# Performance work log

Hardware: AMD Instinct MI355X
Metric: run time of the kernel (lower is better)

Reference implementation:

```python
import jax, jax.numpy as jnp
import numpy as np

B, N, T, IN_DIM, OUT_DIM = 16, 500, 12, 2, 2
H, D, K, NH, NBLOCKS, T_OUT, GDEP = 64, 64, 10, 24, 2, 12, 2
H2 = 2 * H


def setup_inputs():
    key = jax.random.key(0)
    ks = iter(jax.random.split(key, 64))

    def rn(shape, s=1.0):
        return jax.random.normal(next(ks), shape, dtype=jnp.float32) * s

    def z(*shape):
        return jnp.zeros(shape, jnp.float32)

    sI = 1.0 / np.sqrt(IN_DIM)
    sH = 1.0 / np.sqrt(H)
    sH2 = 1.0 / np.sqrt(H2)
    sD = 1.0 / np.sqrt(D)
    adj = jax.random.uniform(next(ks), (N, N), dtype=jnp.float32)
    inp = {
        'x': rn((B, N, T, IN_DIM)),
        'weather': rn((B, T, 4)),
        'geo_adj': adj / adj.sum(1, keepdims=True),
        'fcx_W': rn((IN_DIM, H), sI), 'fcx_b': z(H),
        'env_cb': rn((K, D)), 'nodes_cb': rn((N, D)),
        'w_v': rn((D, K), sD), 'w_k': rn((D, D), sD), 'w_q': rn((D, D), sD),
        'core_W': rn((H, H * H), sH), 'core_b': z(H * H),
        'tcnN_Win': rn((K, H2, H2), sH2), 'tcnN_bin': z(K, H2),
        'tcnN_Wf': rn((K, NBLOCKS, 2, H2, H2), sH2), 'tcnN_bf': z(K, NBLOCKS, H2),
        'tcnN_Wg': rn((K, NBLOCKS, 2, H2, H2), sH2), 'tcnN_bg': z(K, NBLOCKS, H2),
        'tcnN_Wout': rn((K, H2, H), sH2), 'tcnN_bout': z(K, H),
        'tcnP_Win': rn((K, H2, H2), sH2), 'tcnP_bin': z(K, H2),
        'tcnP_Wf': rn((K, NBLOCKS, 2, H2, H2), sH2), 'tcnP_bf': z(K, NBLOCKS, H2),
        'tcnP_Wg': rn((K, NBLOCKS, 2, H2, H2), sH2), 'tcnP_bg': z(K, NBLOCKS, H2),
        'tcnP_Wout': rn((K, H2, H), sH2), 'tcnP_bout': z(K, H),
        'bn1_g': jnp.ones((H,), jnp.float32), 'bn1_b': z(H),
        'bnP_g': jnp.ones((H,), jnp.float32), 'bnP_b': z(H),
        'gcn1_W': rn((H, H), sH), 'gcn1_b': z(H),
        'gcn2_W': rn((H, H), sH), 'gcn2_b': z(H),
        'gcnp_W': rn((H, H), sH), 'gcnp_b': z(H),
        'nv_p1': rn((2 * NH, H)), 'nv_p2': rn((N, H)), 'nv_p3': rn((N, H)),
        'nv_pk': rn((H, H, H), sH),
        'out_W1': rn((T_OUT, H, 100), sH), 'out_b1': z(T_OUT, 100),
        'out_W2': rn((T_OUT, 100, OUT_DIM), 0.1), 'out_b2': z(T_OUT, OUT_DIM),
        't_pos': jax.random.randint(next(ks), (B, T, 2), 0, 7),
        'ind': jax.random.randint(next(ks), (B, T, 2), 0, 7),
    }
    return inp


def _tstep_emb(t, dim):
    half = dim // 2
    freqs = jnp.exp(-jnp.log(10000.0) * jnp.arange(half, dtype=jnp.float32) / half)
    a = t.astype(jnp.float32)[:, None] * freqs[None]
    return jnp.concatenate([jnp.cos(a), jnp.sin(a)], -1)


def _conv2(h, W, b, d):
    # causal kernel-2 dilated conv over time: h [B,N,T,C], W [2,C,Co] -> [B,N,T-d,Co]
    return (jnp.einsum('bntc,co->bnto', h[:, :, :-d], W[0])
            + jnp.einsum('bntc,co->bnto', h[:, :, d:], W[1]) + b)


def _tcn(xin, Win, bin_, Wf, bf, Wg, bg, Wout, bout):
    # gated dilated TCN (Graph-WaveNet style), per node over time
    h = jnp.einsum('bntc,co->bnto', xin, Win) + bin_
    for l in range(Wf.shape[0]):
        d = 2 ** l
        f = jnp.tanh(_conv2(h, Wf[l], bf[l], d))
        g = jax.nn.sigmoid(_conv2(h, Wg[l], bg[l], d))
        h = f * g + h[:, :, d:, :]
    return jnp.einsum('bntc,ch->bnth', h, Wout) + bout


def _bn(h, g, b):
    # BatchNorm1d over channels, stats over (batch, nodes); training mode
    mu = h.mean((0, 1))
    var = h.var((0, 1))
    return g * (h - mu) * jax.lax.rsqrt(var + 1e-5) + b


def _gcn(h, adj, W, b):
    # multi-hop diffusion: sum_{k=0..GDEP} A^k h, then linear
    eq = 'nm,bmh->bnh' if adj.ndim == 2 else 'bnm,bmh->bnh'
    acc, zt = h, h
    for _ in range(GDEP):
        zt = jnp.einsum(eq, adj, zt)
        acc = acc + zt
    return jnp.einsum('bnh,ho->bno', acc, W) + b


def _forward(x, weather, geo_adj, fcx_W, fcx_b, env_cb, nodes_cb, w_v, w_k, w_q,
             core_W, core_b,
             tcnN_Win, tcnN_bin, tcnN_Wf, tcnN_bf, tcnN_Wg, tcnN_bg, tcnN_Wout, tcnN_bout,
             tcnP_Win, tcnP_bin, tcnP_Wf, tcnP_bf, tcnP_Wg, tcnP_bg, tcnP_Wout, tcnP_bout,
             bn1_g, bn1_b, bnP_g, bnP_b, gcn1_W, gcn1_b, gcn2_W, gcn2_b, gcnp_W, gcnp_b,
             nv_p1, nv_p2, nv_p3, nv_pk, out_W1, out_b1, out_W2, out_b2, t_pos, ind):
    scale = 1.0 / jnp.sqrt(jnp.float32(D))
    ind_p = jnp.where(ind[:, :, 0] <= 4, ind[:, :, 1], NH - 1 + ind[:, :, 1])
    tp = jnp.where(t_pos[:, :, 0] <= 4, t_pos[:, :, 1], NH - 1 + t_pos[:, :, 1])
    t_emb = _tstep_emb(tp.reshape(-1), H).reshape(B, T, H)

    # codebook attention -> hard cluster assignment (gumbel softmax, straight-through)
    mat_v = env_cb @ w_v
    mat_k = env_cb @ w_k
    mat_q = nodes_cb @ w_q
    scores = jax.nn.softmax((mat_q @ mat_k.T) * scale, axis=1)
    logits = scores @ mat_v                                   # [N,K]
    gn = jax.random.gumbel(jax.random.key(42), logits.shape, dtype=logits.dtype)
    y_soft = jax.nn.softmax(logits + gn, axis=1)
    hard = jax.nn.one_hot(jnp.argmax(y_soft, axis=1), K, dtype=y_soft.dtype)
    mask = y_soft + jax.lax.stop_gradient(hard - y_soft)      # [N,K] one-hot fwd

    x_emb = jnp.einsum('bnti,ih->bnth', x, fcx_W) + fcx_b
    total_x = jnp.concatenate(
        [x_emb, jnp.broadcast_to(t_emb[:, None], (B, N, T, H))], -1)  # [B,N,T,2H]

    unbias = jnp.zeros((B, N, H), total_x.dtype)
    h_prev = jnp.zeros((B, N, H), total_x.dtype)
    for i in range(K):  # small fixed cluster count
        m = mask[:, i]
        xm = total_x * m[None, :, None, None]
        hn = _tcn(xm[:, :, 1:], tcnN_Win[i], tcnN_bin[i], tcnN_Wf[i], tcnN_bf[i],
                  tcnN_Wg[i], tcnN_bg[i], tcnN_Wout[i], tcnN_bout[i])[:, :, 0, :]
        hp = _tcn(xm[:, :, :-1], tcnP_Win[i], tcnP_bin[i], tcnP_Wf[i], tcnP_bf[i],
                  tcnP_Wg[i], tcnP_bg[i], tcnP_Wout[i], tcnP_bout[i])[:, :, 0, :]
        unbias = unbias + m[None, :, None] * hn
        h_prev = h_prev + m[None, :, None] * hp

    unbias = _bn(unbias, bn1_g, bn1_b)
    h_prev = _bn(h_prev, bnP_g, bnP_b)

    h1 = _gcn(h_prev, geo_adj, gcn1_W, gcn1_b)
    core = (t_emb[:, T - 1] @ core_W + core_b).reshape(B, H, H)
    causal = jax.nn.softmax(jnp.einsum('bnh,bhk,bmk->bnm', unbias, core, h_prev), axis=-1)
    h2 = _gcn(unbias, causal, gcn2_W, gcn2_b)

    te = nv_p1[ind_p[:, -(T - 1)]]                            # [B,H]
    adp = jnp.einsum('ai,ijk->ajk', te, nv_pk)
    adp = jnp.einsum('bj,ajk->abk', nv_p2, adp)
    adp = jnp.einsum('ck,abk->abc', nv_p3, adp)
    adp = jax.nn.softmax(jax.nn.relu(adp), axis=2)            # [B,N,N]
    h3 = _gcn(unbias, adp, gcnp_W, gcnp_b)

    cur_h = h1 + h2 + h3
    hmid = jax.nn.elu(jnp.einsum('bnh,thf->bntf', cur_h, out_W1) + out_b1)
    return jnp.einsum('bntf,tfo->bnto', hmid, out_W2) + out_b2  # [B,N,T_OUT,OUT_DIM]


def reference(x, weather, geo_adj, fcx_W, fcx_b, env_cb, nodes_cb, w_v, w_k, w_q,
              core_W, core_b,
              tcnN_Win, tcnN_bin, tcnN_Wf, tcnN_bf, tcnN_Wg, tcnN_bg, tcnN_Wout, tcnN_bout,
              tcnP_Win, tcnP_bin, tcnP_Wf, tcnP_bf, tcnP_Wg, tcnP_bg, tcnP_Wout, tcnP_bout,
              bn1_g, bn1_b, bnP_g, bnP_b, gcn1_W, gcn1_b, gcn2_W, gcn2_b, gcnp_W, gcnp_b,
              nv_p1, nv_p2, nv_p3, nv_pk, out_W1, out_b1, out_W2, out_b2, t_pos, ind):
    return _forward(x, weather, geo_adj, fcx_W, fcx_b, env_cb, nodes_cb, w_v, w_k, w_q,
                    core_W, core_b,
                    tcnN_Win, tcnN_bin, tcnN_Wf, tcnN_bf, tcnN_Wg, tcnN_bg, tcnN_Wout, tcnN_bout,
                    tcnP_Win, tcnP_bin, tcnP_Wf, tcnP_bf, tcnP_Wg, tcnP_bg, tcnP_Wout, tcnP_bout,
                    bn1_g, bn1_b, bnP_g, bnP_b, gcn1_W, gcn1_b, gcn2_W, gcn2_b, gcnp_W, gcnp_b,
                    nv_p1, nv_p2, nv_p3, nv_pk, out_W1, out_b1, out_W2, out_b2, t_pos, ind)
```

## Files before the change

kernel.cpp:

```cpp
#include <hip/hip_runtime.h>
#include <hip/hip_bf16.h>
#include <math.h>

#define B_ 16
#define N_ 500
#define T_ 12
#define K_ 10
#define NROWS (B_*N_)
#define TROWS 6

__device__ __forceinline__ unsigned rotl32(unsigned v, int r){ return (v<<r)|(v>>(32-r)); }

__device__ __forceinline__ void threefry2x32(unsigned k0, unsigned k1,
                                             unsigned c0, unsigned c1,
                                             unsigned &o0, unsigned &o1){
  unsigned ks2 = k0 ^ k1 ^ 0x1BD11BDAu;
  unsigned x0 = c0 + k0, x1 = c1 + k1;
#define TF_R(r) { x0 += x1; x1 = rotl32(x1,(r)); x1 ^= x0; }
  TF_R(13) TF_R(15) TF_R(26) TF_R(6)
  x0 += k1;  x1 += ks2 + 1u;
  TF_R(17) TF_R(29) TF_R(16) TF_R(24)
  x0 += ks2; x1 += k0 + 2u;
  TF_R(13) TF_R(15) TF_R(26) TF_R(6)
  x0 += k0;  x1 += k1 + 3u;
// ... 481 lines not shown
    #pragma unroll
    for (int ii=0;ii<3;++ii){
      int i = ig + ii;
      float f = tanhf(af[ii] + bfv);
      float g = 1.f/(1.f + expf(-(ag[ii] + bgv)));
      sH2[i*128 + o] = f*g + sH1[(i*2+1)*128 + o];
    }
  }
  __syncthreads();

  {
    int o6 = tid & 63, grp = tid >> 6;
    #pragma unroll
    for (int ii=0; ii<2; ++ii){
      int i = grp*2 + ii;
      if (i >= TROWS) continue;
      float acc = 0.f;
      for (int c = 0; c < 128; c += 4){
        float w0=Wout[(c+0)*64+o6], w1=Wout[(c+1)*64+o6],
              w2=Wout[(c+2)*64+o6], w3=Wout[(c+3)*64+o6];
        float4 xv = *(const float4*)&sH2[i*128 + c];
        acc += xv.x*w0 + xv.y*w1 + xv.z*w2 + xv.w*w3;
      }
      if (rowBN[i] >= 0) outb[rowBN[i]*64 + o6] = acc + bout[o6];
    }
  }
}

__global__ __launch_bounds__(256) void k_bnstats(const float* __restrict__ unb,
                                                 const float* __restrict__ hpr,
                                                 float* __restrict__ stats){
  int bid = blockIdx.x;
  int tensor = bid >> 6, c = bid & 63;
  const float* buf = tensor ? hpr : unb;
  float s1 = 0.f, s2 = 0.f;
  for (int r = threadIdx.x; r < NROWS; r += 256){
    float v = buf[r*64 + c];
    s1 += v; s2 += v*v;
  }
  __shared__ float r1[256], r2[256];
  r1[threadIdx.x]=s1; r2[threadIdx.x]=s2;
  __syncthreads();
  for (int s=128; s>0; s>>=1){
    if (threadIdx.x < s){ r1[threadIdx.x]+=r1[threadIdx.x+s]; r2[threadIdx.x]+=r2[threadIdx.x+s]; }
    __syncthreads();
  }
  if (threadIdx.x==0){
    float mean = r1[0]/(float)NROWS;
    float var  = r2[0]/(float)NROWS - mean*mean;
    stats[tensor*128 + c]      = mean;
    stats[tensor*128 + 64 + c] = rsqrtf(var + 1e-5f);
  }
}

__global__ __launch_bounds__(256) void k_bnapply(float* __restrict__ unb, float* __restrict__ hpr,
                                                 const float* __restrict__ stats,
                                                 const float* __restrict__ g1, const float* __restrict__ be1,
                                                 const float* __restrict__ gP, const float* __restrict__ beP){
  int idx = blockIdx.x*256 + threadIdx.x;
  if (idx >= 2*NROWS*64) return;
  int tensor = idx >= NROWS*64;
  int local = idx - tensor*NROWS*64;
  int c = local & 63;
  float* buf = tensor ? hpr : unb;
  float mean = stats[tensor*128+c], rstd = stats[tensor*128+64+c];
  float g = tensor ? gP[c] : g1[c];
  float bb = tensor ? beP[c] : be1[c];
  buf[local] = g * (buf[local]-mean) * rstd + bb;
}

template<int AMODE, int RELU, int FINAL, int ADD>
__global__ __launch_bounds__(256) void k_attn(
    const float* __restrict__ geo,
    const float* __restrict__ Qf, const float* __restrict__ Qb,
    const float* __restrict__ M,
    const float* __restrict__ Keysf, const float* __restrict__ Keysb,
    const float* __restrict__ X,
    const float* __restrict__ X0, const float* __restrict__ Z1,
    const float* __restrict__ Wg, const float* __restrict__ bg,
    float* __restrict__ cur, float* __restrict__ Y)
{
  __shared__ __align__(16) float kbuf[64][65];
  __shared__ __align__(16) float xbuf[64][64];
  __shared__ __align__(16) float vbuf[8][64];
  __shared__ __align__(16) float pbuf[8][64];

  int b = blockIdx.y, n0 = blockIdx.x*8;
  int tid = threadIdx.x;
  int nl = tid >> 5, ml = tid & 31;
  int n = n0 + nl;
  float rrK[16], rrX[16], rrA[2];

  if (AMODE != 0){
    for (int idx = tid; idx < 512; idx += 256){
      int r = idx >> 6, kk = idx & 63;
      int nn = n0 + r;
      float q = 0.f;
      if (nn < N_) q = (AMODE == 1) ? Qf[(b*N_+nn)*64+kk] : Qb[nn*64+kk];
      pbuf[r][kk] = q;
    }
    for (int idx = tid; idx < 4096; idx += 256)
      kbuf[idx>>6][idx&63] = M[b*4096 + idx];
    __syncthreads();
    float vx = 0.f, vy = 0.f;
    for (int kk = 0; kk < 64; ++kk){
      float q = pbuf[nl][kk];
      float2 m2 = *(const float2*)&kbuf[kk][ml*2];
      vx += q*m2.x; vy += q*m2.y;
    }
    __syncthreads();
    vbuf[nl][ml*2]   = vx;
    vbuf[nl][ml*2+1] = vy;
  }
  {
    if (AMODE != 0) __syncthreads();
    #pragma unroll
    for (int ii = 0; ii < 16; ++ii){
      int idx = tid + ii*256;
      int mm = idx >> 6, kk = idx & 63;
      if (AMODE != 0)
        kbuf[mm][kk] = (AMODE == 1) ? Keysf[(b*N_+mm)*64+kk] : Keysb[mm*64+kk];
      xbuf[mm][kk] = X[(b*N_+mm)*64+kk];
    }
    if (AMODE == 0){
      #pragma unroll
      for (int ii = 0; ii < 2; ++ii){
        int idx = tid + ii*256;
        int r = idx >> 6, mm = idx & 63;
        int nn = n0 + r;
        pbuf[r][mm] = (nn < N_) ? geo[nn*N_ + mm] : 0.f;
      }
    }
    __syncthreads();
  }

  float m_run = -1e30f, l_run = 0.f;
  float accx = 0.f, accy = 0.f;

  for (int ci = 0; ci < 8; ++ci){
    int m0 = ci*64;
    if (ci < 7){
      #pragma unroll
      for (int ii=0; ii<16; ++ii){
        int idx = tid + ii*256;
        int mm = idx >> 6, kk = idx & 63;
        int m = m0 + 64 + mm;
        if (AMODE != 0)
          rrK[ii] = (m < N_) ? ((AMODE == 1) ? Keysf[(b*N_+m)*64+kk] : Keysb[m*64+kk]) : 0.f;
        rrX[ii] = (m < N_) ? X[(b*N_+m)*64+kk] : 0.f;
      }
      if (AMODE == 0){
        #pragma unroll
        for (int ii=0; ii<2; ++ii){
          int idx = tid + ii*256;
          int r = idx >> 6, mm = idx & 63;
          int nn = n0 + r, m = m0 + 64 + mm;
          rrA[ii] = (nn < N_ && m < N_) ? geo[nn*N_ + m] : 0.f;
        }
      }
    }
    if (AMODE != 0){
      float s0 = 0.f, s1 = 0.f;
      for (int kk = 0; kk < 64; kk += 4){
        float4 qv = *(const float4*)&vbuf[nl][kk];
        float4 k0 = *(const float4*)&kbuf[ml   ][kk];
        float4 k1 = *(const float4*)&kbuf[ml+32][kk];
        s0 += qv.x*k0.x + qv.y*k0.y + qv.z*k0.z + qv.w*k0.w;
        s1 += qv.x*k1.x + qv.y*k1.y + qv.z*k1.z + qv.w*k1.w;
      }
      float v0 = (m0 + ml      < N_) ? (RELU ? fmaxf(s0, 0.f) : s0) : -1e30f;
      float v1 = (m0 + ml + 32 < N_) ? (RELU ? fmaxf(s1, 0.f) : s1) : -1e30f;
      float cmax = fmaxf(v0, v1);
      #pragma unroll
      for (int msk = 1; msk < 32; msk <<= 1) cmax = fmaxf(cmax, __shfl_xor(cmax, msk, 32));
      float mnew = fmaxf(m_run, cmax);
      float scale = expf(m_run - mnew);
      float p0 = expf(v0 - mnew);
      float p1 = expf(v1 - mnew);
      float lc = p0 + p1;
      #pragma unroll
      for (int msk = 1; msk < 32; msk <<= 1) lc += __shfl_xor(lc, msk, 32);
      l_run = l_run*scale + lc;
      m_run = mnew;
      accx *= scale; accy *= scale;
      pbuf[nl][ml]    = p0;
      pbuf[nl][ml+32] = p1;
    }
    __syncthreads();
    for (int mm = 0; mm < 64; mm += 4){
      float4 pv = *(const float4*)&pbuf[nl][mm];
      float2 x0 = *(const float2*)&xbuf[mm+0][ml*2];
      float2 x1 = *(const float2*)&xbuf[mm+1][ml*2];
      float2 x2 = *(const float2*)&xbuf[mm+2][ml*2];
      float2 x3 = *(const float2*)&xbuf[mm+3][ml*2];
      accx += pv.x*x0.x + pv.y*x1.x + pv.z*x2.x + pv.w*x3.x;
      accy += pv.x*x0.y + pv.y*x1.y + pv.z*x2.y + pv.w*x3.y;
    }
    __syncthreads();
    if (ci < 7){
      #pragma unroll
      for (int ii=0; ii<16; ++ii){
        int idx = tid + ii*256;
        int mm = idx >> 6, kk = idx & 63;
        if (AMODE != 0) kbuf[mm][kk] = rrK[ii];
        xbuf[mm][kk] = rrX[ii];
      }
      if (AMODE == 0){
        #pragma unroll
        for (int ii=0; ii<2; ++ii){
          int idx = tid + ii*256;
          pbuf[idx>>6][idx&63] = rrA[ii];
        }
      }
      __syncthreads();
    }
  }
  if (AMODE != 0){
    float inv = 1.f / l_run;
    accx *= inv; accy *= inv;
  }

  if (!FINAL){
    if (n < N_){
      float2 o2; o2.x = accx; o2.y = accy;
      *(float2*)&Y[(b*N_+n)*64 + ml*2] = o2;
    }
    return;
  }

  {
    int row = b*N_ + n;
    float svx = 0.f, svy = 0.f;
    if (n < N_){
      float2 x0v = *(const float2*)&X0[row*64 + ml*2];
      float2 z1v = *(const float2*)&Z1[row*64 + ml*2];
      svx = accx + x0v.x + z1v.x;
      svy = accy + x0v.y + z1v.y;
    }
    vbuf[nl][ml*2]   = svx;
    vbuf[nl][ml*2+1] = svy;
    for (int idx = tid; idx < 4096; idx += 256)
      kbuf[idx>>6][idx&63] = Wg[idx];
    __syncthreads();
    float ox = 0.f, oy = 0.f;
    for (int kk = 0; kk < 64; ++kk){
      float s = vbuf[nl][kk];
      float2 w2 = *(const float2*)&kbuf[kk][ml*2];
      ox += s*w2.x; oy += s*w2.y;
    }
    if (n < N_){
      float2 bv = *(const float2*)&bg[ml*2];
      float vx = ox + bv.x, vy = oy + bv.y;
      if (ADD){
        float2 old = *(const float2*)&cur[row*64 + ml*2];
        vx += old.x; vy += old.y;
      }
      float2 o2; o2.x = vx; o2.y = vy;
      *(float2*)&cur[row*64 + ml*2] = o2;
    }
  }
}

template<int AMODE, int RELU>
__global__ __launch_bounds__(256) void k_attn_p1(
    const float* __restrict__ Qf, const float* __restrict__ Qb,
    const float* __restrict__ M,
    const float* __restrict__ Keysf, const float* __restrict__ Keysb,
    const float* __restrict__ X,
    float* __restrict__ Pb, float* __restrict__ Y)
{
  __shared__ __align__(16) float kbuf[64][65];
  __shared__ __align__(16) float xbuf[64][64];
  __shared__ __align__(16) float vbuf[8][64];
  __shared__ __align__(16) float pbuf[8][64];

  int b = blockIdx.y, n0 = blockIdx.x*8;
  int tid = threadIdx.x;
  int nl = tid >> 5, ml = tid & 31;
  int n = n0 + nl;
  float rrK[16], rrX[16];

  for (int idx = tid; idx < 512; idx += 256){
    int r = idx >> 6, kk = idx & 63;
    int nn = n0 + r;
    float q = 0.f;
    if (nn < N_) q = (AMODE == 1) ? Qf[(b*N_+nn)*64+kk] : Qb[nn*64+kk];
    pbuf[r][kk] = q;
  }
  for (int idx = tid; idx < 4096; idx += 256)
    kbuf[idx>>6][idx&63] = M[b*4096 + idx];
  __syncthreads();
  float vx = 0.f, vy = 0.f;
  for (int kk = 0; kk < 64; ++kk){
    float q = pbuf[nl][kk];
    float2 m2 = *(const float2*)&kbuf[kk][ml*2];
    vx += q*m2.x; vy += q*m2.y;
  }
  __syncthreads();
  vbuf[nl][ml*2]   = vx;
  vbuf[nl][ml*2+1] = vy;
  __syncthreads();
  #pragma unroll
  for (int ii = 0; ii < 16; ++ii){
    int idx = tid + ii*256;
    int mm = idx >> 6, kk = idx & 63;
    kbuf[mm][kk] = (AMODE == 1) ? Keysf[(b*N_+mm)*64+kk] : Keysb[mm*64+kk];
    xbuf[mm][kk] = X[(b*N_+mm)*64+kk];
  }
  __syncthreads();

  float m_run = -1e30f, l_run = 0.f;
  float accx = 0.f, accy = 0.f;

  for (int ci = 0; ci < 8; ++ci){
    int m0 = ci*64;
    if (ci < 7){
      #pragma unroll
      for (int ii=0; ii<16; ++ii){
        int idx = tid + ii*256;
        int mm = idx >> 6, kk = idx & 63;
        int m = m0 + 64 + mm;
        rrK[ii] = (m < N_) ? ((AMODE == 1) ? Keysf[(b*N_+m)*64+kk] : Keysb[m*64+kk]) : 0.f;
        rrX[ii] = (m < N_) ? X[(b*N_+m)*64+kk] : 0.f;
      }
    }
    {
      float s0 = 0.f, s1 = 0.f;
      for (int kk = 0; kk < 64; kk += 4){
        float4 qv = *(const float4*)&vbuf[nl][kk];
        float4 k0 = *(const float4*)&kbuf[ml   ][kk];
        float4 k1 = *(const float4*)&kbuf[ml+32][kk];
        s0 += qv.x*k0.x + qv.y*k0.y + qv.z*k0.z + qv.w*k0.w;
        s1 += qv.x*k1.x + qv.y*k1.y + qv.z*k1.z + qv.w*k1.w;
      }
      float v0 = (m0 + ml      < N_) ? (RELU ? fmaxf(s0, 0.f) : s0) : -1e30f;
      float v1 = (m0 + ml + 32 < N_) ? (RELU ? fmaxf(s1, 0.f) : s1) : -1e30f;
      if (n < N_){
        Pb[((long)(b*N_+n))*512 + m0 + ml]      = v0;
        Pb[((long)(b*N_+n))*512 + m0 + ml + 32] = v1;
      }
      float cmax = fmaxf(v0, v1);
      #pragma unroll
      for (int msk = 1; msk < 32; msk <<= 1) cmax = fmaxf(cmax, __shfl_xor(cmax, msk, 32));
      float mnew = fmaxf(m_run, cmax);
      float scale = expf(m_run - mnew);
      float p0 = expf(v0 - mnew);
      float p1 = expf(v1 - mnew);
      float lc = p0 + p1;
      #pragma unroll
      for (int msk = 1; msk < 32; msk <<= 1) lc += __shfl_xor(lc, msk, 32);
      l_run = l_run*scale + lc;
      m_run = mnew;
      accx *= scale; accy *= scale;
      pbuf[nl][ml]    = p0;
      pbuf[nl][ml+32] = p1;
    }
    __syncthreads();
    for (int mm = 0; mm < 64; mm += 4){
      float4 pv = *(const float4*)&pbuf[nl][mm];
      float2 x0 = *(const float2*)&xbuf[mm+0][ml*2];
      float2 x1 = *(const float2*)&xbuf[mm+1][ml*2];
      float2 x2 = *(const float2*)&xbuf[mm+2][ml*2];
      float2 x3 = *(const float2*)&xbuf[mm+3][ml*2];
      accx += pv.x*x0.x + pv.y*x1.x + pv.z*x2.x + pv.w*x3.x;
      accy += pv.x*x0.y + pv.y*x1.y + pv.z*x2.y + pv.w*x3.y;
    }
    __syncthreads();
    if (ci < 7){
      #pragma unroll
      for (int ii=0; ii<16; ++ii){
        int idx = tid + ii*256;
        kbuf[idx>>6][idx&63] = rrK[ii];
        xbuf[idx>>6][idx&63] = rrX[ii];
      }
      __syncthreads();
    }
  }
  float inv = 1.f / l_run;
  accx *= inv; accy *= inv;
  if (n < N_){
    float2 o2; o2.x = accx; o2.y = accy;
    *(float2*)&Y[(b*N_+n)*64 + ml*2] = o2;
  }
}

template<int ADD>
__global__ __launch_bounds__(256) void k_attn_p2(
    const float* __restrict__ Pb,
    const float* __restrict__ X,
    const float* __restrict__ X0,
    const float* __restrict__ Wg, const float* __restrict__ bg,
    float* __restrict__ cur)
{
  __shared__ __align__(16) float pbuf[8][516];
  __shared__ __align__(16) float xbuf[64][64];
  __shared__ __align__(16) float vbuf[8][64];

  int b = blockIdx.y, n0 = blockIdx.x*8;
  int tid = threadIdx.x;
  int nl = tid >> 5, ml = tid & 31;
  int n = n0 + nl;
  float rrX[16];

  for (int idx = tid; idx < 8*512; idx += 256){
    int r = idx >> 9, m = idx & 511;
    int nn = n0 + r;
    pbuf[r][m] = (nn < N_) ? Pb[((long)(b*N_+nn))*512 + m] : -1e30f;
  }
  __syncthreads();
  float lmax = -1e30f;
  for (int m = ml; m < 512; m += 32) lmax = fmaxf(lmax, pbuf[nl][m]);
  #pragma unroll
  for (int msk=1; msk<32; msk<<=1) lmax = fmaxf(lmax, __shfl_xor(lmax, msk, 32));
  float lsum = 0.f;
  for (int m = ml; m < 512; m += 32){
    float p = expf(pbuf[nl][m] - lmax);
    pbuf[nl][m] = p;
    lsum += p;
  }
  #pragma unroll
  for (int msk=1; msk<32; msk<<=1) lsum += __shfl_xor(lsum, msk, 32);
  float inv = 1.f/lsum;
  for (int m = ml; m < 512; m += 32) pbuf[nl][m] *= inv;

  #pragma unroll
  for (int ii=0; ii<16; ++ii){
    int idx = tid + ii*256;
    int mm = idx>>6, kk = idx&63;
    xbuf[mm][kk] = X[(b*N_+mm)*64+kk];
  }
  __syncthreads();

  float accx = 0.f, accy = 0.f;
  for (int ci = 0; ci < 8; ++ci){
    int m0 = ci*64;
    if (ci < 7){
      #pragma unroll
      for (int ii=0; ii<16; ++ii){
        int idx = tid + ii*256;
        int mm = idx>>6, kk = idx&63;
        int m = m0+64+mm;
        rrX[ii] = (m < N_) ? X[(b*N_+m)*64+kk] : 0.f;
      }
    }
    for (int mm = 0; mm < 64; mm += 4){
      float4 pv = *(const float4*)&pbuf[nl][m0+mm];
      float2 x0 = *(const float2*)&xbuf[mm+0][ml*2];
      float2 x1 = *(const float2*)&xbuf[mm+1][ml*2];
      float2 x2 = *(const float2*)&xbuf[mm+2][ml*2];
      float2 x3 = *(const float2*)&xbuf[mm+3][ml*2];
      accx += pv.x*x0.x + pv.y*x1.x + pv.z*x2.x + pv.w*x3.x;
      accy += pv.x*x0.y + pv.y*x1.y + pv.z*x2.y + pv.w*x3.y;
    }
    __syncthreads();
    if (ci < 7){
      #pragma unroll
      for (int ii=0; ii<16; ++ii){
        int idx = tid + ii*256;
        xbuf[idx>>6][idx&63] = rrX[ii];
      }
      __syncthreads();
    }
  }

  {
    int row = b*N_ + n;
    float svx = 0.f, svy = 0.f;
    if (n < N_){
      float2 x0v = *(const float2*)&X0[row*64 + ml*2];
      float2 z1v = *(const float2*)&X[row*64 + ml*2];
      svx = accx + x0v.x + z1v.x;
      svy = accy + x0v.y + z1v.y;
    }
    vbuf[nl][ml*2]   = svx;
    vbuf[nl][ml*2+1] = svy;
    for (int idx = tid; idx < 4096; idx += 256)
      xbuf[idx>>6][idx&63] = Wg[idx];
    __syncthreads();
    float ox = 0.f, oy = 0.f;
    for (int kk = 0; kk < 64; ++kk){
      float s = vbuf[nl][kk];
      float2 w2 = *(const float2*)&xbuf[kk][ml*2];
      ox += s*w2.x; oy += s*w2.y;
    }
    if (n < N_){
      float2 bv = *(const float2*)&bg[ml*2];
      float vx = ox + bv.x, vy = oy + bv.y;
      if (ADD){
        float2 old = *(const float2*)&cur[row*64 + ml*2];
        vx += old.x; vy += old.y;
      }
      float2 o2; o2.x = vx; o2.y = vy;
      *(float2*)&cur[row*64 + ml*2] = o2;
    }
  }
}

__global__ __launch_bounds__(128) void k_out(const float* __restrict__ cur,
                                             const float* __restrict__ W1, const float* __restrict__ bb1,
                                             const float* __restrict__ W2, const float* __restrict__ bb2,
                                             float* __restrict__ out){
  __shared__ float ch[4][64];
  __shared__ float hid[4*1200];
  int tid = threadIdx.x;
  int rbase = blockIdx.x*4;
  for (int idx = tid; idx < 256; idx += 128){
    int r = idx >> 6, h = idx & 63;
    ch[r][h] = cur[(rbase+r)*64 + h];
  }
  __syncthreads();
  for (int job = tid; job < 1200; job += 128){
    int t = job / 100, f = job - t*100;
    float a0 = bb1[t*100+f], a1 = a0, a2 = a0, a3 = a0;
    for (int h = 0; h < 64; ++h){
      float w = W1[(t*64+h)*100 + f];
      a0 += ch[0][h]*w; a1 += ch[1][h]*w; a2 += ch[2][h]*w; a3 += ch[3][h]*w;
    }
    hid[0*1200+job] = (a0 > 0.f) ? a0 : expm1f(a0);
    hid[1*1200+job] = (a1 > 0.f) ? a1 : expm1f(a1);
    hid[2*1200+job] = (a2 > 0.f) ? a2 : expm1f(a2);
    hid[3*1200+job] = (a3 > 0.f) ? a3 : expm1f(a3);
  }
  __syncthreads();
  if (tid < 96){
    int r = tid / 24, rem = tid % 24;
    int t = rem >> 1, o = rem & 1;
    float a = bb2[t*2+o];
    const float* hp = hid + r*1200 + t*100;
    for (int f = 0; f < 100; ++f) a += hp[f] * W2[(t*100+f)*2+o];
    out[(rbase+r)*24 + t*2+o] = a;
  }
}

extern "C" void kernel_launch(void* const* d_in, const int* in_sizes, int n_in,
                              void* d_out, int out_size, void* d_ws, size_t ws_size,
                              hipStream_t stream)
{
  const float* x        = (const float*)d_in[0];
  const float* geo      = (const float*)d_in[2];
  const float* fcx_W    = (const float*)d_in[3];
  const float* fcx_b    = (const float*)d_in[4];
  const float* env_cb   = (const float*)d_in[5];
  const float* nodes_cb = (const float*)d_in[6];
  const float* w_v      = (const float*)d_in[7];
  const float* w_k      = (const float*)d_in[8];
  const float* w_q      = (const float*)d_in[9];
  const float* core_W   = (const float*)d_in[10];
  const float* core_b   = (const float*)d_in[11];
  const float* tN_Win   = (const float*)d_in[12];
  const float* tN_bin   = (const float*)d_in[13];
  const float* tN_Wf    = (const float*)d_in[14];
  const float* tN_bf    = (const float*)d_in[15];
  const float* tN_Wg    = (const float*)d_in[16];
  const float* tN_bg    = (const float*)d_in[17];
  const float* tN_Wout  = (const float*)d_in[18];
  const float* tN_bout  = (const float*)d_in[19];
  const float* tP_Win   = (const float*)d_in[20];
  const float* tP_bin   = (const float*)d_in[21];
  const float* tP_Wf    = (const float*)d_in[22];
  const float* tP_bf    = (const float*)d_in[23];
  const float* tP_Wg    = (const float*)d_in[24];
  const float* tP_bg    = (const float*)d_in[25];
  const float* tP_Wout  = (const float*)d_in[26];
  const float* tP_bout  = (const float*)d_in[27];
  const float* bn1_g    = (const float*)d_in[28];
  const float* bn1_b    = (const float*)d_in[29];
  const float* bnP_g    = (const float*)d_in[30];
  const float* bnP_b    = (const float*)d_in[31];
  const float* gcn1_W   = (const float*)d_in[32];
  const float* gcn1_b   = (const float*)d_in[33];
  const float* gcn2_W   = (const float*)d_in[34];
  const float* gcn2_b   = (const float*)d_in[35];
  const float* gcnp_W   = (const float*)d_in[36];
  const float* gcnp_b   = (const float*)d_in[37];
  const float* nv_p1    = (const float*)d_in[38];
  const float* nv_p2    = (const float*)d_in[39];
  const float* nv_p3    = (const float*)d_in[40];
  const float* nv_pk    = (const float*)d_in[41];
  const float* out_W1   = (const float*)d_in[42];
  const float* out_b1   = (const float*)d_in[43];
  const float* out_W2   = (const float*)d_in[44];
  const float* out_b2   = (const float*)d_in[45];
  const int*   t_pos    = (const int*)d_in[46];
  const int*   ind      = (const int*)d_in[47];

  int* node_list = (int*)d_ws;
  int* off       = node_list + 512;
  float* F = (float*)((char*)d_ws + 4096);
  float* temb   = F + 0;
  float* core_f = F + 12288;
  float* tmp1   = F + 77824;
  float* stats  = F + 143360;
  float* matq   = F + 143616;
  float* unb    = F + 175616;
  float* hpr    = F + 687616;
  float* cur    = F + 1199616;
  float* zt1    = F + 1711616;
  float* Pb     = F + 2223616;
  float* TE     = Pb;
  bool useP = ws_size >= (size_t)(4096 + (size_t)(2223616 + 4096000)*4);

  k_matq <<<dim3(125), dim3(256), 0, stream>>>(nodes_cb, w_q, matq);
  k_route<<<dim3(1),   dim3(256), 0, stream>>>(env_cb, w_v, w_k, matq, node_list, off);
  k_temb <<<dim3(1),   dim3(192), 0, stream>>>(t_pos, temb);
  k_core <<<dim3(256), dim3(256), 0, stream>>>(temb, core_W, core_b, core_f);
  if (useP){
    k_tprep<<<dim3(20, 81), dim3(128), 0, stream>>>(temb, fcx_W, fcx_b, tN_Win, tP_Win, TE);
    k_tcn2 <<<dim3(20, 334), dim3(256), 0, stream>>>(x, TE, node_list, off,
        tN_bin, tN_Wf, tN_bf, tN_Wg, tN_bg, tN_Wout, tN_bout,
        tP_bin, tP_Wf, tP_bf, tP_Wg, tP_bg, tP_Wout, tP_bout,
        unb, hpr);
  } else {
    k_tcn  <<<dim3(20, 334), dim3(256), 0, stream>>>(x, fcx_W, fcx_b, temb, node_list, off,
        tN_Win, tN_bin, tN_Wf, tN_bf, tN_Wg, tN_bg, tN_Wout, tN_bout,
        tP_Win, tP_bin, tP_Wf, tP_bf, tP_Wg, tP_bg, tP_Wout, tP_bout,
        unb, hpr);
  }
  k_bnstats<<<dim3(128), dim3(256), 0, stream>>>(unb, hpr, stats);
  k_bnapply<<<dim3(4000),dim3(256), 0, stream>>>(unb, hpr, stats, bn1_g, bn1_b, bnP_g, bnP_b);
  k_tmp1<<<dim3(256), dim3(256), 0, stream>>>(ind, nv_p1, nv_pk, tmp1);

  dim3 ag(64, 16);
  const float* nil = nullptr;
  k_attn<0,0,0,0><<<ag, 256, 0, stream>>>(geo, nil,nil,nil, nil,nil,
                                 hpr, nil,nil, nil,nil, nullptr, zt1);
  k_attn<0,0,1,0><<<ag, 256, 0, stream>>>(geo, nil,nil,nil, nil,nil,
                                 zt1, hpr, zt1, gcn1_W, gcn1_b, cur, nullptr);
  if (useP){
    k_attn_p1<1,0><<<ag, 256, 0, stream>>>(unb, nil, core_f, hpr, nil, unb, Pb, zt1);
    k_attn_p2<1>  <<<ag, 256, 0, stream>>>(Pb, zt1, unb, gcn2_W, gcn2_b, cur);
  } else {
    k_attn<1,0,0,0><<<ag, 256, 0, stream>>>(nil, unb,nil, core_f, hpr,nil,
                                   unb, nil,nil, nil,nil, nullptr, zt1);
    k_attn<1,0,1,1><<<ag, 256, 0, stream>>>(nil, unb,nil, core_f, hpr,nil,
                                   zt1, unb, zt1, gcn2_W, gcn2_b, cur, nullptr);
  }
  if (useP){
    k_attn_p1<2,1><<<ag, 256, 0, stream>>>(nil, nv_p2, tmp1, nil, nv_p3, unb, Pb, zt1);
    k_attn_p2<1>  <<<ag, 256, 0, stream>>>(Pb, zt1, unb, gcnp_W, gcnp_b, cur);
  } else {
    k_attn<2,1,0,0><<<ag, 256, 0, stream>>>(nil, nil,nv_p2, tmp1, nil,nv_p3,
                                   unb, nil,nil, nil,nil, nullptr, zt1);
    k_attn<2,1,1,1><<<ag, 256, 0, stream>>>(nil, nil,nv_p2, tmp1, nil,nv_p3,
                                   zt1, unb, zt1, gcnp_W, gcnp_b, cur, nullptr);
  }
  k_out<<<dim3(2000), dim3(128), 0, stream>>>(cur, out_W1, out_b1, out_W2, out_b2, (float*)d_out);
}
```

Baseline: 950.8 us.

## Process two query rows per warp in attention kernels to reuse key/value tiles

Each block of the attention kernels (k_attn, k_attn_p1, k_attn_p2) now covers 16 query nodes instead of 8, with every warp handling two rows (A and B). This halves the grid and reuses each staged key/X chunk from shared memory for twice as many queries, which cuts global loads of keys and values per output. In exchange it raises register pressure and shared memory per block and launches fewer blocks (32x16), which may lower occupancy.

```diff
diff --git a/kernel.cpp b/kernel.cpp
--- a/kernel.cpp
+++ b/kernel.cpp
@@ -587,17 +587,17 @@
 {
   __shared__ __align__(16) float kbuf[64][65];
   __shared__ __align__(16) float xbuf[64][64];
-  __shared__ __align__(16) float vbuf[8][64];
-  __shared__ __align__(16) float pbuf[8][64];
-
-  int b = blockIdx.y, n0 = blockIdx.x*8;
+  __shared__ __align__(16) float vbuf[16][64];
+  __shared__ __align__(16) float pbuf[16][64];
+
+  int b = blockIdx.y, n0 = blockIdx.x*16;
   int tid = threadIdx.x;
   int nl = tid >> 5, ml = tid & 31;
-  int n = n0 + nl;
-  float rrK[16], rrX[16], rrA[2];
+  int nA = n0 + nl, nB = n0 + nl + 8;
+  float rrK[16], rrX[16], rrA[4];
 
   if (AMODE != 0){
-    for (int idx = tid; idx < 512; idx += 256){
+    for (int idx = tid; idx < 1024; idx += 256){
       int r = idx >> 6, kk = idx & 63;
       int nn = n0 + r;
       float q = 0.f;
@@ -607,15 +607,16 @@
     for (int idx = tid; idx < 4096; idx += 256)
       kbuf[idx>>6][idx&63] = M[b*4096 + idx];
     __syncthreads();
-    float vx = 0.f, vy = 0.f;
+    float vxA = 0.f, vyA = 0.f, vxB = 0.f, vyB = 0.f;
     for (int kk = 0; kk < 64; ++kk){
-      float q = pbuf[nl][kk];
+      float qA = pbuf[nl][kk], qB = pbuf[nl+8][kk];
       float2 m2 = *(const float2*)&kbuf[kk][ml*2];
-      vx += q*m2.x; vy += q*m2.y;
+      vxA += qA*m2.x; vyA += qA*m2.y;
+      vxB += qB*m2.x; vyB += qB*m2.y;
     }
     __syncthreads();
-    vbuf[nl][ml*2]   = vx;
-    vbuf[nl][ml*2+1] = vy;
+    vbuf[nl  ][ml*2] = vxA; vbuf[nl  ][ml*2+1] = vyA;
+    vbuf[nl+8][ml*2] = vxB; vbuf[nl+8][ml*2+1] = vyB;
   }
   {
     if (AMODE != 0) __syncthreads();
@@ -629,7 +630,7 @@
     }
     if (AMODE == 0){
       #pragma unroll
-      for (int ii = 0; ii < 2; ++ii){
+      for (int ii = 0; ii < 4; ++ii){
         int idx = tid + ii*256;
         int r = idx >> 6, mm = idx & 63;
         int nn = n0 + r;
@@ -639,8 +640,9 @@
     __syncthreads();
   }
 
-  float m_run = -1e30f, l_run = 0.f;
-  float accx = 0.f, accy = 0.f;
+  float m_runA = -1e30f, l_runA = 0.f;
+  float m_runB = -1e30f, l_runB = 0.f;
+  float accxA = 0.f, accyA = 0.f, accxB = 0.f, accyB = 0.f;
 
   for (int ci = 0; ci < 8; ++ci){
     int m0 = ci*64;
@@ -656,7 +658,7 @@
       }
       if (AMODE == 0){
         #pragma unroll
-        for (int ii=0; ii<2; ++ii){
+        for (int ii=0; ii<4; ++ii){
           int idx = tid + ii*256;
           int r = idx >> 6, mm = idx & 63;
           int nn = n0 + r, m = m0 + 64 + mm;
@@ -665,41 +667,58 @@
       }
     }
     if (AMODE != 0){
-      float s0 = 0.f, s1 = 0.f;
+      float s0A = 0.f, s1A = 0.f, s0B = 0.f, s1B = 0.f;
       for (int kk = 0; kk < 64; kk += 4){
-        float4 qv = *(const float4*)&vbuf[nl][kk];
+        float4 qA = *(const float4*)&vbuf[nl  ][kk];
+        float4 qB = *(const float4*)&vbuf[nl+8][kk];
         float4 k0 = *(const float4*)&kbuf[ml   ][kk];
         float4 k1 = *(const float4*)&kbuf[ml+32][kk];
-        s0 += qv.x*k0.x + qv.y*k0.y + qv.z*k0.z + qv.w*k0.w;
-        s1 += qv.x*k1.x + qv.y*k1.y + qv.z*k1.z + qv.w*k1.w;
-      }
-      float v0 = (m0 + ml      < N_) ? (RELU ? fmaxf(s0, 0.f) : s0) : -1e30f;
-      float v1 = (m0 + ml + 32 < N_) ? (RELU ? fmaxf(s1, 0.f) : s1) : -1e30f;
-      float cmax = fmaxf(v0, v1);
-      #pragma unroll
-      for (int msk = 1; msk < 32; msk <<= 1) cmax = fmaxf(cmax, __shfl_xor(cmax, msk, 32));
-      float mnew = fmaxf(m_run, cmax);
-      float scale = expf(m_run - mnew);
-      float p0 = expf(v0 - mnew);
-      float p1 = expf(v1 - mnew);
-      float lc = p0 + p1;
-      #pragma unroll
-      for (int msk = 1; msk < 32; msk <<= 1) lc += __shfl_xor(lc, msk, 32);
-      l_run = l_run*scale + lc;
-      m_run = mnew;
-      accx *= scale; accy *= scale;
-      pbuf[nl][ml]    = p0;
-      pbuf[nl][ml+32] = p1;
+        s0A += qA.x*k0.x + qA.y*k0.y + qA.z*k0.z + qA.w*k0.w;
+        s1A += qA.x*k1.x + qA.y*k1.y + qA.z*k1.z + qA.w*k1.w;
+        s0B += qB.x*k0.x + qB.y*k0.y + qB.z*k0.z + qB.w*k0.w;
+        s1B += qB.x*k1.x + qB.y*k1.y + qB.z*k1.z + qB.w*k1.w;
+      }
+      float v0A = (m0 + ml      < N_) ? (RELU ? fmaxf(s0A, 0.f) : s0A) : -1e30f;
+      float v1A = (m0 + ml + 32 < N_) ? (RELU ? fmaxf(s1A, 0.f) : s1A) : -1e30f;
+      float v0B = (m0 + ml      < N_) ? (RELU ? fmaxf(s0B, 0.f) : s0B) : -1e30f;
+      float v1B = (m0 + ml + 32 < N_) ? (RELU ? fmaxf(s1B, 0.f) : s1B) : -1e30f;
+      float cmaxA = fmaxf(v0A, v1A), cmaxB = fmaxf(v0B, v1B);
+      #pragma unroll
+      for (int msk = 1; msk < 32; msk <<= 1){
+        cmaxA = fmaxf(cmaxA, __shfl_xor(cmaxA, msk, 32));
+        cmaxB = fmaxf(cmaxB, __shfl_xor(cmaxB, msk, 32));
+      }
+      float mnewA = fmaxf(m_runA, cmaxA), mnewB = fmaxf(m_runB, cmaxB);
+      float scaleA = expf(m_runA - mnewA), scaleB = expf(m_runB - mnewB);
+      float p0A = expf(v0A - mnewA), p1A = expf(v1A - mnewA);
+      float p0B = expf(v0B - mnewB), p1B = expf(v1B - mnewB);
+      float lcA = p0A + p1A, lcB = p0B + p1B;
+      #pragma unroll
+      for (int msk = 1; msk < 32; msk <<= 1){
+        lcA += __shfl_xor(lcA, msk, 32);
+        lcB += __shfl_xor(lcB, msk, 32);
+      }
+      l_runA = l_runA*scaleA + lcA; m_runA = mnewA;
+      l_runB = l_runB*scaleB + lcB; m_runB = mnewB;
+      accxA *= scaleA; accyA *= scaleA;
+      accxB *= scaleB; accyB *= scaleB;
+      pbuf[nl  ][ml]    = p0A;
+      pbuf[nl  ][ml+32] = p1A;
+      pbuf[nl+8][ml]    = p0B;
+      pbuf[nl+8][ml+32] = p1B;
     }
     __syncthreads();
     for (int mm = 0; mm < 64; mm += 4){
-      float4 pv = *(const float4*)&pbuf[nl][mm];
+      float4 pA = *(const float4*)&pbuf[nl  ][mm];
+      float4 pB = *(const float4*)&pbuf[nl+8][mm];
       float2 x0 = *(const float2*)&xbuf[mm+0][ml*2];
       float2 x1 = *(const float2*)&xbuf[mm+1][ml*2];
       float2 x2 = *(const float2*)&xbuf[mm+2][ml*2];
       float2 x3 = *(const float2*)&xbuf[mm+3][ml*2];
-      accx += pv.x*x0.x + pv.y*x1.x + pv.z*x2.x + pv.w*x3.x;
-      accy += pv.x*x0.y + pv.y*x1.y + pv.z*x2.y + pv.w*x3.y;
+      accxA += pA.x*x0.x + pA.y*x1.x + pA.z*x2.x + pA.w*x3.x;
+      accyA += pA.x*x0.y + pA.y*x1.y + pA.z*x2.y + pA.w*x3.y;
+      accxB += pB.x*x0.x + pB.y*x1.x + pB.z*x2.x + pB.w*x3.x;
+      accyB += pB.x*x0.y + pB.y*x1.y + pB.z*x2.y + pB.w*x3.y;
     }
     __syncthreads();
     if (ci < 7){
@@ -712,7 +731,7 @@
       }
       if (AMODE == 0){
         #pragma unroll
-        for (int ii=0; ii<2; ++ii){
+        for (int ii=0; ii<4; ++ii){
           int idx = tid + ii*256;
           pbuf[idx>>6][idx&63] = rrA[ii];
         }
@@ -721,41 +740,65 @@
     }
   }
   if (AMODE != 0){
-    float inv = 1.f / l_run;
-    accx *= inv; accy *= inv;
+    float invA = 1.f / l_runA, invB = 1.f / l_runB;
+    accxA *= invA; accyA *= invA;
+    accxB *= invB; accyB *= invB;
   }
 
   if (!FINAL){
-    if (n < N_){
-      float2 o2; o2.x = accx; o2.y = accy;
-      *(float2*)&Y[(b*N_+n)*64 + ml*2] = o2;
+    if (nA < N_){
+      float2 o2; o2.x = accxA; o2.y = accyA;
+      *(float2*)&Y[(b*N_+nA)*64 + ml*2] = o2;
+    }
+    if (nB < N_){
+      float2 o2; o2.x = accxB; o2.y = accyB;
+      *(float2*)&Y[(b*N_+nB)*64 + ml*2] = o2;
     }
     return;
   }
 
   {
-    int row = b*N_ + n;
-    float svx = 0.f, svy = 0.f;
-    if (n < N_){
+    float svxA = 0.f, svyA = 0.f, svxB = 0.f, svyB = 0.f;
+    if (nA < N_){
+      int row = b*N_ + nA;
       float2 x0v = *(const float2*)&X0[row*64 + ml*2];
       float2 z1v = *(const float2*)&Z1[row*64 + ml*2];
-      svx = accx + x0v.x + z1v.x;
-      svy = accy + x0v.y + z1v.y;
-    }
-    vbuf[nl][ml*2]   = svx;
-    vbuf[nl][ml*2+1] = svy;
+      svxA = accxA + x0v.x + z1v.x;
+      svyA = accyA + x0v.y + z1v.y;
+    }
+    if (nB < N_){
+      int row = b*N_ + nB;
+      float2 x0v = *(const float2*)&X0[row*64 + ml*2];
+      float2 z1v = *(const float2*)&Z1[row*64 + ml*2];
+      svxB = accxB + x0v.x + z1v.x;
+      svyB = accyB + x0v.y + z1v.y;
+    }
+    vbuf[nl  ][ml*2] = svxA; vbuf[nl  ][ml*2+1] = svyA;
+    vbuf[nl+8][ml*2] = svxB; vbuf[nl+8][ml*2+1] = svyB;
     for (int idx = tid; idx < 4096; idx += 256)
       kbuf[idx>>6][idx&63] = Wg[idx];
     __syncthreads();
-    float ox = 0.f, oy = 0.f;
+    float oxA = 0.f, oyA = 0.f, oxB = 0.f, oyB = 0.f;
     for (int kk = 0; kk < 64; ++kk){
-      float s = vbuf[nl][kk];
+      float sA = vbuf[nl][kk], sB = vbuf[nl+8][kk];
       float2 w2 = *(const float2*)&kbuf[kk][ml*2];
-      ox += s*w2.x; oy += s*w2.y;
-    }
-    if (n < N_){
-      float2 bv = *(const float2*)&bg[ml*2];
-      float vx = ox + bv.x, vy = oy + bv.y;
+      oxA += sA*w2.x; oyA += sA*w2.y;
+      oxB += sB*w2.x; oyB += sB*w2.y;
+    }
+    float2 bv = *(const float2*)&bg[ml*2];
+    if (nA < N_){
+      int row = b*N_ + nA;
+      float vx = oxA + bv.x, vy = oyA + bv.y;
+      if (ADD){
+        float2 old = *(const float2*)&cur[row*64 + ml*2];
+        vx += old.x; vy += old.y;
+      }
+      float2 o2; o2.x = vx; o2.y = vy;
+      *(float2*)&cur[row*64 + ml*2] = o2;
+    }
+    if (nB < N_){
+      int row = b*N_ + nB;
+      float vx = oxB + bv.x, vy = oyB + bv.y;
       if (ADD){
         float2 old = *(const float2*)&cur[row*64 + ml*2];
         vx += old.x; vy += old.y;
@@ -776,16 +819,16 @@
 {
   __shared__ __align__(16) float kbuf[64][65];
   __shared__ __align__(16) float xbuf[64][64];
-  __shared__ __align__(16) float vbuf[8][64];
-  __shared__ __align__(16) float pbuf[8][64];
-
-  int b = blockIdx.y, n0 = blockIdx.x*8;
+  __shared__ __align__(16) float vbuf[16][64];
+  __shared__ __align__(16) float pbuf[16][64];
+
+  int b = blockIdx.y, n0 = blockIdx.x*16;
   int tid = threadIdx.x;
   int nl = tid >> 5, ml = tid & 31;
-  int n = n0 + nl;
+  int nA = n0 + nl, nB = n0 + nl + 8;
   float rrK[16], rrX[16];
 
-  for (int idx = tid; idx < 512; idx += 256){
+  for (int idx = tid; idx < 1024; idx += 256){
     int r = idx >> 6, kk = idx & 63;
     int nn = n0 + r;
     float q = 0.f;
@@ -795,15 +838,16 @@
   for (int idx = tid; idx < 4096; idx += 256)
     kbuf[idx>>6][idx&63] = M[b*4096 + idx];
   __syncthreads();
-  float vx = 0.f, vy = 0.f;
+  float vxA = 0.f, vyA = 0.f, vxB = 0.f, vyB = 0.f;
   for (int kk = 0; kk < 64; ++kk){
-    float q = pbuf[nl][kk];
+    float qA = pbuf[nl][kk], qB = pbuf[nl+8][kk];
     float2 m2 = *(const float2*)&kbuf[kk][ml*2];
-    vx += q*m2.x; vy += q*m2.y;
-  }
-  __syncthreads();
-  vbuf[nl][ml*2]   = vx;
-  vbuf[nl][ml*2+1] = vy;
+    vxA += qA*m2.x; vyA += qA*m2.y;
+    vxB += qB*m2.x; vyB += qB*m2.y;
+  }
+  __syncthreads();
+  vbuf[nl  ][ml*2] = vxA; vbuf[nl  ][ml*2+1] = vyA;
+  vbuf[nl+8][ml*2] = vxB; vbuf[nl+8][ml*2+1] = vyB;
   __syncthreads();
   #pragma unroll
   for (int ii = 0; ii < 16; ++ii){
@@ -814,8 +858,9 @@
   }
   __syncthreads();
 
-  float m_run = -1e30f, l_run = 0.f;
-  float accx = 0.f, accy = 0.f;
+  float m_runA = -1e30f, l_runA = 0.f;
+  float m_runB = -1e30f, l_runB = 0.f;
+  float accxA = 0.f, accyA = 0.f, accxB = 0.f, accyB = 0.f;
 
   for (int ci = 0; ci < 8; ++ci){
     int m0 = ci*64;
@@ -830,45 +875,66 @@
       }
     }
     {
-      float s0 = 0.f, s1 = 0.f;
+      float s0A = 0.f, s1A = 0.f, s0B = 0.f, s1B = 0.f;
       for (int kk = 0; kk < 64; kk += 4){
-        float4 qv = *(const float4*)&vbuf[nl][kk];
+        float4 qA = *(const float4*)&vbuf[nl  ][kk];
+        float4 qB = *(const float4*)&vbuf[nl+8][kk];
         float4 k0 = *(const float4*)&kbuf[ml   ][kk];
         float4 k1 = *(const float4*)&kbuf[ml+32][kk];
-        s0 += qv.x*k0.x + qv.y*k0.y + qv.z*k0.z + qv.w*k0.w;
-        s1 += qv.x*k1.x + qv.y*k1.y + qv.z*k1.z + qv.w*k1.w;
-      }
-      float v0 = (m0 + ml      < N_) ? (RELU ? fmaxf(s0, 0.f) : s0) : -1e30f;
-      float v1 = (m0 + ml + 32 < N_) ? (RELU ? fmaxf(s1, 0.f) : s1) : -1e30f;
-      if (n < N_){
-        Pb[((long)(b*N_+n))*512 + m0 + ml]      = v0;
-        Pb[((long)(b*N_+n))*512 + m0 + ml + 32] = v1;
-      }
-      float cmax = fmaxf(v0, v1);
-      #pragma unroll
-      for (int msk = 1; msk < 32; msk <<= 1) cmax = fmaxf(cmax, __shfl_xor(cmax, msk, 32));
-      float mnew = fmaxf(m_run, cmax);
-      float scale = expf(m_run - mnew);
-      float p0 = expf(v0 - mnew);
-      float p1 = expf(v1 - mnew);
-      float lc = p0 + p1;
-      #pragma unroll
-      for (int msk = 1; msk < 32; msk <<= 1) lc += __shfl_xor(lc, msk, 32);
-      l_run = l_run*scale + lc;
-      m_run = mnew;
-      accx *= scale; accy *= scale;
-      pbuf[nl][ml]    = p0;
-      pbuf[nl][ml+32] = p1;
+        s0A += qA.x*k0.x + qA.y*k0.y + qA.z*k0.z + qA.w*k0.w;
+        s1A += qA.x*k1.x + qA.y*k1.y + qA.z*k1.z + qA.w*k1.w;
+        s0B += qB.x*k0.x + qB.y*k0.y + qB.z*k0.z + qB.w*k0.w;
+        s1B += qB.x*k1.x + qB.y*k1.y + qB.z*k1.z + qB.w*k1.w;
+      }
+      float v0A = (m0 + ml      < N_) ? (RELU ? fmaxf(s0A, 0.f) : s0A) : -1e30f;
+      float v1A = (m0 + ml + 32 < N_) ? (RELU ? fmaxf(s1A, 0.f) : s1A) : -1e30f;
+      float v0B = (m0 + ml      < N_) ? (RELU ? fmaxf(s0B, 0.f) : s0B) : -1e30f;
+      float v1B = (m0 + ml + 32 < N_) ? (RELU ? fmaxf(s1B, 0.f) : s1B) : -1e30f;
+      if (nA < N_){
+        Pb[((long)(b*N_+nA))*512 + m0 + ml]      = v0A;
+        Pb[((long)(b*N_+nA))*512 + m0 + ml + 32] = v1A;
+      }
+      if (nB < N_){
+        Pb[((long)(b*N_+nB))*512 + m0 + ml]      = v0B;
+        Pb[((long)(b*N_+nB))*512 + m0 + ml + 32] = v1B;
+      }
+      float cmaxA = fmaxf(v0A, v1A), cmaxB = fmaxf(v0B, v1B);
+      #pragma unroll
+      for (int msk = 1; msk < 32; msk <<= 1){
+        cmaxA = fmaxf(cmaxA, __shfl_xor(cmaxA, msk, 32));
+        cmaxB = fmaxf(cmaxB, __shfl_xor(cmaxB, msk, 32));
+      }
+      float mnewA = fmaxf(m_runA, cmaxA), mnewB = fmaxf(m_runB, cmaxB);
+      float scaleA = expf(m_runA - mnewA), scaleB = expf(m_runB - mnewB);
+      float p0A = expf(v0A - mnewA), p1A = expf(v1A - mnewA);
+      float p0B = expf(v0B - mnewB), p1B = expf(v1B - mnewB);
+      float lcA = p0A + p1A, lcB = p0B + p1B;
+      #pragma unroll
+      for (int msk = 1; msk < 32; msk <<= 1){
+        lcA += __shfl_xor(lcA, msk, 32);
+        lcB += __shfl_xor(lcB, msk, 32);
+      }
+      l_runA = l_runA*scaleA + lcA; m_runA = mnewA;
+      l_runB = l_runB*scaleB + lcB; m_runB = mnewB;
+      accxA *= scaleA; accyA *= scaleA;
+      accxB *= scaleB; accyB *= scaleB;
+      pbuf[nl  ][ml]    = p0A;
+      pbuf[nl  ][ml+32] = p1A;
+      pbuf[nl+8][ml]    = p0B;
+      pbuf[nl+8][ml+32] = p1B;
     }
     __syncthreads();
     for (int mm = 0; mm < 64; mm += 4){
-      float4 pv = *(const float4*)&pbuf[nl][mm];
+      float4 pA = *(const float4*)&pbuf[nl  ][mm];
+      float4 pB = *(const float4*)&pbuf[nl+8][mm];
       float2 x0 = *(const float2*)&xbuf[mm+0][ml*2];
       float2 x1 = *(const float2*)&xbuf[mm+1][ml*2];
       float2 x2 = *(const float2*)&xbuf[mm+2][ml*2];
       float2 x3 = *(const float2*)&xbuf[mm+3][ml*2];
-      accx += pv.x*x0.x + pv.y*x1.x + pv.z*x2.x + pv.w*x3.x;
-      accy += pv.x*x0.y + pv.y*x1.y + pv.z*x2.y + pv.w*x3.y;
+      accxA += pA.x*x0.x + pA.y*x1.x + pA.z*x2.x + pA.w*x3.x;
+      accyA += pA.x*x0.y + pA.y*x1.y + pA.z*x2.y + pA.w*x3.y;
+      accxB += pB.x*x0.x + pB.y*x1.x + pB.z*x2.x + pB.w*x3.x;
+      accyB += pB.x*x0.y + pB.y*x1.y + pB.z*x2.y + pB.w*x3.y;
     }
     __syncthreads();
     if (ci < 7){
@@ -881,11 +947,16 @@
       __syncthreads();
     }
   }
-  float inv = 1.f / l_run;
-  accx *= inv; accy *= inv;
-  if (n < N_){
-    float2 o2; o2.x = accx; o2.y = accy;
-    *(float2*)&Y[(b*N_+n)*64 + ml*2] = o2;
+  float invA = 1.f / l_runA, invB = 1.f / l_runB;
+  accxA *= invA; accyA *= invA;
+  accxB *= invB; accyB *= invB;
+  if (nA < N_){
+    float2 o2; o2.x = accxA; o2.y = accyA;
+    *(float2*)&Y[(b*N_+nA)*64 + ml*2] = o2;
+  }
+  if (nB < N_){
+    float2 o2; o2.x = accxB; o2.y = accyB;
+    *(float2*)&Y[(b*N_+nB)*64 + ml*2] = o2;
   }
 }
 
@@ -897,36 +968,50 @@
     const float* __restrict__ Wg, const float* __restrict__ bg,
     float* __restrict__ cur)
 {
-  __shared__ __align__(16) float pbuf[8][516];
+  __shared__ __align__(16) float pbuf[16][516];
   __shared__ __align__(16) float xbuf[64][64];
-  __shared__ __align__(16) float vbuf[8][64];
-
-  int b = blockIdx.y, n0 = blockIdx.x*8;
+  __shared__ __align__(16) float vbuf[16][64];
+
+  int b = blockIdx.y, n0 = blockIdx.x*16;
   int tid = threadIdx.x;
   int nl = tid >> 5, ml = tid & 31;
-  int n = n0 + nl;
+  int nA = n0 + nl, nB = n0 + nl + 8;
   float rrX[16];
 
-  for (int idx = tid; idx < 8*512; idx += 256){
+  for (int idx = tid; idx < 16*512; idx += 256){
     int r = idx >> 9, m = idx & 511;
     int nn = n0 + r;
     pbuf[r][m] = (nn < N_) ? Pb[((long)(b*N_+nn))*512 + m] : -1e30f;
   }
   __syncthreads();
-  float lmax = -1e30f;
-  for (int m = ml; m < 512; m += 32) lmax = fmaxf(lmax, pbuf[nl][m]);
+  float lmaxA = -1e30f, lmaxB = -1e30f;
+  for (int m = ml; m < 512; m += 32){
+    lmaxA = fmaxf(lmaxA, pbuf[nl  ][m]);
+    lmaxB = fmaxf(lmaxB, pbuf[nl+8][m]);
+  }
   #pragma unroll
-  for (int msk=1; msk<32; msk<<=1) lmax = fmaxf(lmax, __shfl_xor(lmax, msk, 32));
-  float lsum = 0.f;
+  for (int msk=1; msk<32; msk<<=1){
+    lmaxA = fmaxf(lmaxA, __shfl_xor(lmaxA, msk, 32));
+    lmaxB = fmaxf(lmaxB, __shfl_xor(lmaxB, msk, 32));
+  }
+  float lsumA = 0.f, lsumB = 0.f;
   for (int m = ml; m < 512; m += 32){
-    float p = expf(pbuf[nl][m] - lmax);
-    pbuf[nl][m] = p;
-    lsum += p;
+    float pA = expf(pbuf[nl  ][m] - lmaxA);
+    float pB = expf(pbuf[nl+8][m] - lmaxB);
+    pbuf[nl  ][m] = pA;
+    pbuf[nl+8][m] = pB;
+    lsumA += pA; lsumB += pB;
   }
   #pragma unroll
-  for (int msk=1; msk<32; msk<<=1) lsum += __shfl_xor(lsum, msk, 32);
-  float inv = 1.f/lsum;
-  for (int m = ml; m < 512; m += 32) pbuf[nl][m] *= inv;
+  for (int msk=1; msk<32; msk<<=1){
+    lsumA += __shfl_xor(lsumA, msk, 32);
+    lsumB += __shfl_xor(lsumB, msk, 32);
+  }
+  float invA = 1.f/lsumA, invB = 1.f/lsumB;
+  for (int m = ml; m < 512; m += 32){
+    pbuf[nl  ][m] *= invA;
+    pbuf[nl+8][m] *= invB;
+  }
 
   #pragma unroll
   for (int ii=0; ii<16; ++ii){
@@ -936,7 +1021,7 @@
   }
   __syncthreads();
 
-  float accx = 0.f, accy = 0.f;
+  float accxA = 0.f, accyA = 0.f, accxB = 0.f, accyB = 0.f;
   for (int ci = 0; ci < 8; ++ci){
     int m0 = ci*64;
     if (ci < 7){
@@ -949,13 +1034,16 @@
       }
     }
     for (int mm = 0; mm < 64; mm += 4){
-      float4 pv = *(const float4*)&pbuf[nl][m0+mm];
+      float4 pA = *(const float4*)&pbuf[nl  ][m0+mm];
+      float4 pB = *(const float4*)&pbuf[nl+8][m0+mm];
       float2 x0 = *(const float2*)&xbuf[mm+0][ml*2];
       float2 x1 = *(const float2*)&xbuf[mm+1][ml*2];
       float2 x2 = *(const float2*)&xbuf[mm+2][ml*2];
       float2 x3 = *(const float2*)&xbuf[mm+3][ml*2];
-      accx += pv.x*x0.x + pv.y*x1.x + pv.z*x2.x + pv.w*x3.x;
-      accy += pv.x*x0.y + pv.y*x1.y + pv.z*x2.y + pv.w*x3.y;
+      accxA += pA.x*x0.x + pA.y*x1.x + pA.z*x2.x + pA.w*x3.x;
+      accyA += pA.x*x0.y + pA.y*x1.y + pA.z*x2.y + pA.w*x3.y;
+      accxB += pB.x*x0.x + pB.y*x1.x + pB.z*x2.x + pB.w*x3.x;
+      accyB += pB.x*x0.y + pB.y*x1.y + pB.z*x2.y + pB.w*x3.y;
     }
     __syncthreads();
     if (ci < 7){
@@ -969,28 +1057,47 @@
   }
 
   {
-    int row = b*N_ + n;
-    float svx = 0.f, svy = 0.f;
-    if (n < N_){
+    float svxA = 0.f, svyA = 0.f, svxB = 0.f, svyB = 0.f;
+    if (nA < N_){
+      int row = b*N_ + nA;
       float2 x0v = *(const float2*)&X0[row*64 + ml*2];
       float2 z1v = *(const float2*)&X[row*64 + ml*2];
-      svx = accx + x0v.x + z1v.x;
-      svy = accy + x0v.y + z1v.y;
-    }
-    vbuf[nl][ml*2]   = svx;
-    vbuf[nl][ml*2+1] = svy;
+      svxA = accxA + x0v.x + z1v.x;
+      svyA = accyA + x0v.y + z1v.y;
+    }
+    if (nB < N_){
+      int row = b*N_ + nB;
+      float2 x0v = *(const float2*)&X0[row*64 + ml*2];
+      float2 z1v = *(const float2*)&X[row*64 + ml*2];
+      svxB = accxB + x0v.x + z1v.x;
+      svyB = accyB + x0v.y + z1v.y;
+    }
+    vbuf[nl  ][ml*2] = svxA; vbuf[nl  ][ml*2+1] = svyA;
+    vbuf[nl+8][ml*2] = svxB; vbuf[nl+8][ml*2+1] = svyB;
     for (int idx = tid; idx < 4096; idx += 256)
       xbuf[idx>>6][idx&63] = Wg[idx];
     __syncthreads();
-    float ox = 0.f, oy = 0.f;
+    float oxA = 0.f, oyA = 0.f, oxB = 0.f, oyB = 0.f;
     for (int kk = 0; kk < 64; ++kk){
-      float s = vbuf[nl][kk];
+      float sA = vbuf[nl][kk], sB = vbuf[nl+8][kk];
       float2 w2 = *(const float2*)&xbuf[kk][ml*2];
-      ox += s*w2.x; oy += s*w2.y;
-    }
-    if (n < N_){
-      float2 bv = *(const float2*)&bg[ml*2];
-      float vx = ox + bv.x, vy = oy + bv.y;
+      oxA += sA*w2.x; oyA += sA*w2.y;
+      oxB += sB*w2.x; oyB += sB*w2.y;
+    }
+    float2 bv = *(const float2*)&bg[ml*2];
+    if (nA < N_){
+      int row = b*N_ + nA;
+      float vx = oxA + bv.x, vy = oyA + bv.y;
+      if (ADD){
+        float2 old = *(const float2*)&cur[row*64 + ml*2];
+        vx += old.x; vy += old.y;
+      }
+      float2 o2; o2.x = vx; o2.y = vy;
+      *(float2*)&cur[row*64 + ml*2] = o2;
+    }
+    if (nB < N_){
+      int row = b*N_ + nB;
+      float vx = oxB + bv.x, vy = oyB + bv.y;
       if (ADD){
         float2 old = *(const float2*)&cur[row*64 + ml*2];
         vx += old.x; vy += old.y;
@@ -1125,7 +1232,7 @@
   k_bnapply<<<dim3(4000),dim3(256), 0, stream>>>(unb, hpr, stats, bn1_g, bn1_b, bnP_g, bnP_b);
   k_tmp1<<<dim3(256), dim3(256), 0, stream>>>(ind, nv_p1, nv_pk, tmp1);
 
-  dim3 ag(64, 16);
+  dim3 ag(32, 16);
   const float* nil = nullptr;
   k_attn<0,0,0,0><<<ag, 256, 0, stream>>>(geo, nil,nil,nil, nil,nil,
                                  hpr, nil,nil, nil,nil, nullptr, zt1);
```

Result: faster. 927.7 us (-2.4%).
